# Kernel optimization log

Hardware: AMD Instinct MI355X
Metric: run time of the kernel (lower is better)

The kernel has to match this reference:

```python
import jax, jax.numpy as jnp
import numpy as np

B, N, D_IN = 4, 2048, 768
D_OUT, H = 768, 12
HD = D_OUT // H  # 64


def setup_inputs() -> dict:
    key = jax.random.key(0)
    ks = jax.random.split(key, 6)
    s = 0.02
    return {
        "x": jax.random.normal(ks[0], (B, N, D_IN), dtype=jnp.float32),
        "W_q": jax.random.normal(ks[1], (D_IN, D_OUT), dtype=jnp.float32) * s,
        "W_k": jax.random.normal(ks[2], (D_IN, D_OUT), dtype=jnp.float32) * s,
        "W_v": jax.random.normal(ks[3], (D_IN, D_OUT), dtype=jnp.float32) * s,
        "W_o": jax.random.normal(ks[4], (D_OUT, D_OUT), dtype=jnp.float32) * s,
        "b_o": jax.random.normal(ks[5], (D_OUT,), dtype=jnp.float32) * s,
    }


def reference(x, W_q, W_k, W_v, W_o, b_o):
    b, n, _ = x.shape
    # project and split heads: [b, h, n, hd]
    q = (x @ W_q).reshape(b, n, H, HD).transpose(0, 2, 1, 3)
    k = (x @ W_k).reshape(b, n, H, HD).transpose(0, 2, 1, 3)
    v = (x @ W_v).reshape(b, n, H, HD).transpose(0, 2, 1, 3)
    scores = jnp.einsum("bhqd,bhkd->bhqk", q, k)
    causal = jnp.tril(jnp.ones((n, n), dtype=bool))
    scores = jnp.where(causal, scores, -jnp.inf)
    w = jax.nn.softmax(scores / jnp.sqrt(jnp.float32(HD)), axis=-1)
    ctx = jnp.einsum("bhqk,bhkd->bhqd", w, v)
    ctx = ctx.transpose(0, 2, 1, 3).reshape(b, n, D_OUT)
    return ctx @ W_o + b_o
```

## Files before the change

kernel.cpp:

```cpp
#include <hip/hip_runtime.h>
#include <hip/hip_bf16.h>
#include <stdint.h>

typedef unsigned short u16;
typedef __attribute__((ext_vector_type(8))) short short8;
typedef __attribute__((ext_vector_type(4))) float f32x4;
typedef __attribute__((ext_vector_type(16))) float f32x16;

#define GLOBAL_AS __attribute__((address_space(1)))
#define LDS_AS __attribute__((address_space(3)))

#define BB 4
#define NSEQ 2048
#define DIN 768
#define DOUT 768
#define NH 12
#define HD 64
#define MROWS (BB*NSEQ)

static __device__ __forceinline__ u16 f2bf(float f) {
  union { float f; uint32_t u; } v; v.f = f;
  uint32_t r = (v.u + 0x7fffu + ((v.u >> 16) & 1u)) >> 16;
  return (u16)r;
}
static __device__ __forceinline__ uint32_t pack2b(float lo, float hi) {
  union { __hip_bfloat162 h; uint32_t u; } cv;
  cv.h.x = __float2bfloat16(lo);
  cv.h.y = __float2bfloat16(hi);
  return cv.u;
}

__global__ __launch_bounds__(256) void convert2_k(const float* __restrict__ x,
                          const float* __restrict__ Wq, const float* __restrict__ Wk,
                          const float* __restrict__ Wv, const float* __restrict__ Wo,
                          u16* __restrict__ xb, u16* __restrict__ WqT,
                          u16* __restrict__ WkT, u16* __restrict__ WvT,
                          u16* __restrict__ WoT) {
  int tid = threadIdx.x;
  if (blockIdx.x < 576) {
    int wi = blockIdx.x;
    int which = wi / 144, t = wi % 144;
    int tr = t / 12, tc = t % 12;
    const float* src = which==0 ? Wq : which==1 ? Wk : which==2 ? Wv : Wo;
    u16* dst = which==0 ? WqT : which==1 ? WkT : which==2 ? WvT : WoT;
    __shared__ u16 lt[64][65];
    int r0 = tid >> 6, c = tid & 63;
#pragma unroll
    for (int rr=0; rr<16; rr++) {
      int row = rr*4 + r0;
      lt[row][c] = f2bf(src[(size_t)(tr*64+row)*DOUT + tc*64 + c]);
    }
    __syncthreads();
#pragma unroll
    for (int rr=0; rr<16; rr++) {
      int row = rr*4 + r0;
      dst[(size_t)(tc*64+row)*DIN + tr*64 + c] = lt[c][row];
    }
  } else {
    const float4* x4 = (const float4*)x;
    uint2* o4 = (uint2*)xb;
    int n4 = MROWS*DIN/4;
    int i = (int)(blockIdx.x - 576) * 256 + tid;
    for (; i < n4; i += 2048*256) {
      float4 v = x4[i];
      uint2 o; o.x = pack2b(v.x, v.y); o.y = pack2b(v.z, v.w);
      o4[i] = o;
    }
  }
}

__global__ __launch_bounds__(256) void gemm_qkv_k(const u16* __restrict__ A,
                                                  const u16* __restrict__ Bt,
                                                  u16* __restrict__ Qg,
                                                  u16* __restrict__ Kgo,
                                                  u16* __restrict__ Vto) {
  const int K = DIN;
  int xcd = blockIdx.x & 7, j = blockIdx.x >> 3;
  int m0 = (xcd*8 + (j & 7)) * 128;
  int n0 = (j >> 3) * 128;
  int tid = threadIdx.x;
  int lane = tid & 63, wid = tid >> 6;
  int wr = wid >> 1, wc = wid & 1;
  int g = lane >> 4, r = lane & 15;

  __shared__ __attribute__((aligned(16))) u16 sbuf[128*129];
  u16* lA = sbuf;
  u16* lB = sbuf + 4096;

  f32x4 acc[4][4];
#pragma unroll
  for (int i=0;i<4;i++)
#pragma unroll
    for (int jj=0;jj<4;jj++) acc[i][jj] = (f32x4){0.f,0.f,0.f,0.f};

  for (int k0 = 0; k0 < K; k0 += 32) {
#pragma unroll
    for (int i=0;i<2;i++) {
      int ch = wid*2 + i;
      int e = ch*512 + lane*8;
      int row = e >> 5, col = e & 31;
      __builtin_amdgcn_global_load_lds(
        (GLOBAL_AS void*)(A + (size_t)(m0+row)*K + k0 + col),
        (LDS_AS void*)(&lA[ch*512]), 16, 0, 0);
      __builtin_amdgcn_global_load_lds(
        (GLOBAL_AS void*)(Bt + (size_t)(n0+row)*K + k0 + col),
        (LDS_AS void*)(&lB[ch*512]), 16, 0, 0);
    }
    __syncthreads();
    short8 af[4], bf[4];
#pragma unroll
    for (int f=0; f<4; f++) {
      af[f] = *(const short8*)&lA[(wr*64 + f*16 + r)*32 + g*8];
      bf[f] = *(const short8*)&lB[(wc*64 + f*16 + r)*32 + g*8];
    }
#pragma unroll
    for (int fr=0; fr<4; fr++)
#pragma unroll
      for (int fc=0; fc<4; fc++)
        acc[fr][fc] = __builtin_amdgcn_mfma_f32_16x16x32_bf16(af[fr], bf[fc], acc[fr][fc], 0, 0, 0);
    __syncthreads();
  }

  if (n0 < 1536) {
    bool isQ = n0 < 768;
    u16* outb = isQ ? Qg : Kgo;
    int nb = isQ ? n0 : n0 - 768;
#pragma unroll
    for (int fr=0; fr<4; fr++)
#pragma unroll
      for (int fc=0; fc<4; fc++)
#pragma unroll
        for (int v=0; v<4; v++) {
          int row = m0 + wr*64 + fr*16 + g*4 + v;
          int cc  = nb + wc*64 + fc*16 + r;
          int b = row >> 11, nn = row & (NSEQ-1);
          float val = acc[fr][fc][v];
          if (isQ) val *= 0.18033688f;
          outb[(((size_t)b*NH + (cc>>6))*NSEQ + nn)*HD + (cc&63)] = f2bf(val);
        }
  } else {
    int nb = n0 - 1536;
#pragma unroll
    for (int fr=0; fr<4; fr++)
#pragma unroll
      for (int fc=0; fc<4; fc++)
#pragma unroll
        for (int v=0; v<4; v++) {
          int ii = wr*64 + fr*16 + g*4 + v;
          int jj = wc*64 + fc*16 + r;
          sbuf[ii*129 + jj] = f2bf(acc[fr][fc][v]);
        }
    __syncthreads();
    int b = m0 >> 11;
#pragma unroll 1
    for (int rep=0; rep<64; rep++) {
      int flat = rep*256 + tid;
      int jj = flat >> 7, ii = flat & 127;
      int cc = nb + jj;
      int nn = (m0 + ii) & (NSEQ-1);
      Vto[(((size_t)b*NH + (cc>>6))*HD + (cc&63))*NSEQ + nn] = sbuf[ii*129 + jj];
    }
  }
}

__global__ __launch_bounds__(256) void gemm_o_k(const u16* __restrict__ A,
                                                const u16* __restrict__ Bt,
                                                float* __restrict__ outf,
                                                const float* __restrict__ bias) {
  const int K = DIN;
  int xcd = blockIdx.x & 7, j = blockIdx.x >> 3;
  int m0 = (xcd*8 + (j & 7)) * 128;
  int n0 = (j >> 3) * 128;
  int tid = threadIdx.x;
  int lane = tid & 63, wid = tid >> 6;
  int wr = wid >> 1, wc = wid & 1;
  int g = lane >> 4, r = lane & 15;

  __shared__ __attribute__((aligned(16))) u16 lA[128*32];
  __shared__ __attribute__((aligned(16))) u16 lB[128*32];

  f32x4 acc[4][4];
#pragma unroll
  for (int i=0;i<4;i++)
#pragma unroll
    for (int jj=0;jj<4;jj++) acc[i][jj] = (f32x4){0.f,0.f,0.f,0.f};

  for (int k0 = 0; k0 < K; k0 += 32) {
#pragma unroll
    for (int i=0;i<2;i++) {
      int ch = wid*2 + i;
      int e = ch*512 + lane*8;
      int row = e >> 5, col = e & 31;
      __builtin_amdgcn_global_load_lds(
        (GLOBAL_AS void*)(A + (size_t)(m0+row)*K + k0 + col),
        (LDS_AS void*)(&lA[ch*512]), 16, 0, 0);
      __builtin_amdgcn_global_load_lds(
        (GLOBAL_AS void*)(Bt + (size_t)(n0+row)*K + k0 + col),
        (LDS_AS void*)(&lB[ch*512]), 16, 0, 0);
    }
    __syncthreads();
    short8 af[4], bf[4];
#pragma unroll
    for (int f=0; f<4; f++) {
      af[f] = *(const short8*)&lA[(wr*64 + f*16 + r)*32 + g*8];
      bf[f] = *(const short8*)&lB[(wc*64 + f*16 + r)*32 + g*8];
    }
#pragma unroll
    for (int fr=0; fr<4; fr++)
#pragma unroll
      for (int fc=0; fc<4; fc++)
        acc[fr][fc] = __builtin_amdgcn_mfma_f32_16x16x32_bf16(af[fr], bf[fc], acc[fr][fc], 0, 0, 0);
    __syncthreads();
  }

#pragma unroll
  for (int fr=0; fr<4; fr++)
#pragma unroll
    for (int fc=0; fc<4; fc++)
#pragma unroll
      for (int v=0; v<4; v++) {
        int row = m0 + wr*64 + fr*16 + g*4 + v;
        int cc  = n0 + wc*64 + fc*16 + r;
        outf[(size_t)row*DOUT + cc] = acc[fr][fc][v] + bias[cc];
      }
}

__global__ __launch_bounds__(256, 4) void attn7_k(const u16* __restrict__ Q,
                                                  const u16* __restrict__ Kg,
                                                  const u16* __restrict__ Vt,
                                                  u16* __restrict__ ctx) {
  int i = blockIdx.x;
  int xcd = i & 7, j = i >> 3;
  int bh = xcd * 6 + (j >> 5);
  int chunk = 31 - (j & 31);
  int nkt = chunk + 1;
  int lane = threadIdx.x & 63;
  int w = threadIdx.x >> 6;
  int p = w >> 1;
  int ch = w & 1;
  int col = lane & 31;
  int hi = lane >> 5;
  int sw = (col & 7) << 4;

  const u16* Qb = Q  + (size_t)bh * NSEQ * HD;
  const u16* Kb = Kg + (size_t)bh * NSEQ * HD;
  const u16* Vb = Vt + (size_t)bh * HD * NSEQ;

  __shared__ __attribute__((aligned(16))) char smem[2][16384];

  auto stage = [&](int buf, int k0) {
#pragma unroll
    for (int ii=0; ii<2; ii++) {
      int cb = (w*2+ii) * 1024;
      int d  = cb + lane*16;
      int row = d >> 7;
      int src = (d & 127) ^ ((row & 7) << 4);
      __builtin_amdgcn_global_load_lds(
        (GLOBAL_AS void*)((const char*)Kb + (size_t)(k0+row)*128 + src),
        (LDS_AS void*)(&smem[buf][cb]), 16, 0, 0);
      __builtin_amdgcn_global_load_lds(
        (GLOBAL_AS void*)((const char*)Vb + (size_t)row*(NSEQ*2) + (size_t)k0*2 + src),
        (LDS_AS void*)(&smem[buf][8192+cb]), 16, 0, 0);
    }
  };

  int qw0 = chunk*64 + p*32;
  int q = qw0 + col;

  short8 qf[4];
#pragma unroll
  for (int ksl = 0; ksl < 4; ksl++)
    qf[ksl] = *(const short8*)&Qb[(size_t)q * HD + ksl*16 + hi*8];

  short8 ones8;
#pragma unroll
  for (int z=0; z<8; z++) ones8[z] = (short)0x3F80;

  f32x16 od[2], ol;
#pragma unroll
  for (int z=0; z<16; z++) { od[0][z] = 0.f; od[1][z] = 0.f; ol[z] = 0.f; }

  stage(0, 0);

#pragma unroll 1
  for (int t = 0; t < nkt; t++) {
    asm volatile("s_waitcnt vmcnt(0)" ::: "memory");
    __builtin_amdgcn_s_barrier();
    asm volatile("" ::: "memory");

    if (t + 1 < nkt) stage((t+1) & 1, (t+1)*64);

    int k0c = t*64 + ch*32;
    if (k0c <= qw0 + 31) {
      const char* Kt = &smem[t & 1][0];
      const char* Vtile = &smem[t & 1][8192];
      f32x16 s;
#pragma unroll
      for (int z=0; z<16; z++) s[z] = 0.f;
#pragma unroll
      for (int ksl=0; ksl<4; ksl++) {
        short8 kf = *(const short8*)(Kt + (ch*32+col)*128 + ((ksl*32 + hi*16) ^ sw));
        s = __builtin_amdgcn_mfma_f32_32x32x16_bf16(kf, qf[ksl], s, 0, 0, 0);
      }
      if (k0c + 31 > qw0) {
#pragma unroll
        for (int r2=0; r2<16; r2++) {
          int kv = k0c + (r2&3) + 8*(r2>>2) + 4*hi;
          if (kv > q) s[r2] = -1e30f;
        }
      }
      uint32_t a[8];
#pragma unroll
      for (int ww=0; ww<8; ww++) {
        float p0 = __builtin_amdgcn_exp2f(s[2*ww]);
        float p1 = __builtin_amdgcn_exp2f(s[2*ww+1]);
        a[ww] = pack2b(p0, p1);
      }

      uint32_t b[8];
#pragma unroll
      for (int ww=0; ww<8; ww++) b[ww] = (uint32_t)__shfl_xor((int)a[ww], 32);
      union { uint32_t wdat[4]; short8 s8; } u0, u1;
      u0.wdat[0] = hi ? b[2]   : a[0];
      u0.wdat[1] = hi ? b[3]   : a[1];
      u0.wdat[2] = hi ? a[2]   : b[0];
      u0.wdat[3] = hi ? a[3]   : b[1];
      u1.wdat[0] = hi ? b[6]   : a[4];
      u1.wdat[1] = hi ? b[7]   : a[5];
      u1.wdat[2] = hi ? a[6]   : b[4];
      u1.wdat[3] = hi ? a[7]   : b[5];
#pragma unroll
      for (int dc=0; dc<2; dc++) {
        short8 vf0 = *(const short8*)(Vtile + (dc*32+col)*128 + ((ch*64 + hi*16) ^ sw));
        od[dc] = __builtin_amdgcn_mfma_f32_32x32x16_bf16(vf0, u0.s8, od[dc], 0, 0, 0);
        short8 vf1 = *(const short8*)(Vtile + (dc*32+col)*128 + ((ch*64 + 32 + hi*16) ^ sw));
        od[dc] = __builtin_amdgcn_mfma_f32_32x32x16_bf16(vf1, u1.s8, od[dc], 0, 0, 0);
      }
      ol = __builtin_amdgcn_mfma_f32_32x32x16_bf16(ones8, u0.s8, ol, 0, 0, 0);
      ol = __builtin_amdgcn_mfma_f32_32x32x16_bf16(ones8, u1.s8, ol, 0, 0, 0);
    }
  }
  __syncthreads();

  float* mg = (float*)&smem[0][0] + p * (33*64);
  if (ch) {
#pragma unroll
    for (int dc=0; dc<2; dc++)
#pragma unroll
      for (int jj=0; jj<16; jj++) mg[(dc*16+jj)*64 + lane] = od[dc][jj];
    mg[32*64 + lane] = ol[0];
  }
  __syncthreads();
  if (!ch) {
    float inv = 1.0f / (ol[0] + mg[32*64 + lane]);
    int b = bh / NH, h = bh % NH;
    u16* cp_ = ctx + ((size_t)b * NSEQ + q) * DOUT + h * HD;
#pragma unroll
    for (int dc=0; dc<2; dc++)
#pragma unroll
      for (int t4=0; t4<4; t4++) {
        int d0 = dc*32 + t4*8 + hi*4;
        float v0 = (od[dc][t4*4+0] + mg[(dc*16+t4*4+0)*64 + lane]) * inv;
        float v1 = (od[dc][t4*4+1] + mg[(dc*16+t4*4+1)*64 + lane]) * inv;
        float v2 = (od[dc][t4*4+2] + mg[(dc*16+t4*4+2)*64 + lane]) * inv;
        float v3 = (od[dc][t4*4+3] + mg[(dc*16+t4*4+3)*64 + lane]) * inv;
        *(uint32_t*)(cp_ + d0)     = pack2b(v0, v1);
        *(uint32_t*)(cp_ + d0 + 2) = pack2b(v2, v3);
      }
  }
}

extern "C" void kernel_launch(void* const* d_in, const int* in_sizes, int n_in,
                              void* d_out, int out_size, void* d_ws, size_t ws_size,
                              hipStream_t stream) {
  const float* x   = (const float*)d_in[0];
  const float* Wq  = (const float*)d_in[1];
  const float* Wk  = (const float*)d_in[2];
  const float* Wv  = (const float*)d_in[3];
  const float* Wo  = (const float*)d_in[4];
  const float* bo  = (const float*)d_in[5];
  float* out = (float*)d_out;

  u16* ws  = (u16*)d_ws;
  u16* xb  = ws;
  u16* WqT = xb  + (size_t)MROWS*DIN;
  u16* WkT = WqT + (size_t)DIN*DOUT;
  u16* WvT = WkT + (size_t)DIN*DOUT;
  u16* WoT = WvT + (size_t)DIN*DOUT;
  u16* Qg  = WoT + (size_t)DIN*DOUT;
  u16* Kg  = Qg  + (size_t)MROWS*DOUT;
  u16* Vt  = Kg  + (size_t)MROWS*DOUT;
  u16* ctx = Vt  + (size_t)MROWS*DOUT;

  convert2_k<<<2624, 256, 0, stream>>>(x, Wq, Wk, Wv, Wo, xb, WqT, WkT, WvT, WoT);

  gemm_qkv_k<<<1152, 256, 0, stream>>>(xb, WqT, Qg, Kg, Vt);

  attn7_k<<<1536, 256, 0, stream>>>(Qg, Kg, Vt, ctx);

  gemm_o_k<<<384, 256, 0, stream>>>(ctx, WoT, out, bo);
}
```

Measured before the change: 142.3 us.

## Double-buffer LDS tiles in QKV and output GEMMs, interleave QKV column tiles

Both projection GEMMs now use two LDS buffers, issuing global-to-LDS loads for the next K-slice before computing on the current one, with one barrier per iteration instead of two. The aim is to overlap memory latency with MFMA work. The QKV GEMM also remaps its column-tile index so Q, K and V tiles are interleaved across blocks, which may balance the different epilogues (V is transposed) across the schedule. The cost is doubled LDS footprint for staging, which may reduce occupancy. Correctness depends on the single barrier plus vmcnt wait ordering LDS reuse properly.

```diff
diff --git a/kernel.cpp b/kernel.cpp
--- a/kernel.cpp
+++ b/kernel.cpp
@@ -77,7 +77,9 @@
   const int K = DIN;
   int xcd = blockIdx.x & 7, j = blockIdx.x >> 3;
   int m0 = (xcd*8 + (j & 7)) * 128;
-  int n0 = (j >> 3) * 128;
+  int nt = j >> 3;
+  nt = (nt % 3) * 6 + nt / 3;
+  int n0 = nt * 128;
   int tid = threadIdx.x;
   int lane = tid & 63, wid = tid >> 6;
   int wr = wid >> 1, wc = wid & 1;
@@ -85,15 +87,9 @@
 
   __shared__ __attribute__((aligned(16))) u16 sbuf[128*129];
   u16* lA = sbuf;
-  u16* lB = sbuf + 4096;
-
-  f32x4 acc[4][4];
-#pragma unroll
-  for (int i=0;i<4;i++)
-#pragma unroll
-    for (int jj=0;jj<4;jj++) acc[i][jj] = (f32x4){0.f,0.f,0.f,0.f};
-
-  for (int k0 = 0; k0 < K; k0 += 32) {
+  u16* lB = sbuf + 8192;
+
+  auto stage = [&](int buf, int k0) {
 #pragma unroll
     for (int i=0;i<2;i++) {
       int ch = wid*2 + i;
@@ -101,25 +97,41 @@
       int row = e >> 5, col = e & 31;
       __builtin_amdgcn_global_load_lds(
         (GLOBAL_AS void*)(A + (size_t)(m0+row)*K + k0 + col),
-        (LDS_AS void*)(&lA[ch*512]), 16, 0, 0);
+        (LDS_AS void*)(&lA[buf*4096 + ch*512]), 16, 0, 0);
       __builtin_amdgcn_global_load_lds(
         (GLOBAL_AS void*)(Bt + (size_t)(n0+row)*K + k0 + col),
-        (LDS_AS void*)(&lB[ch*512]), 16, 0, 0);
-    }
-    __syncthreads();
+        (LDS_AS void*)(&lB[buf*4096 + ch*512]), 16, 0, 0);
+    }
+  };
+
+  f32x4 acc[4][4];
+#pragma unroll
+  for (int i=0;i<4;i++)
+#pragma unroll
+    for (int jj=0;jj<4;jj++) acc[i][jj] = (f32x4){0.f,0.f,0.f,0.f};
+
+  stage(0, 0);
+  int buf = 0;
+  for (int k0 = 0; k0 < K; k0 += 32) {
+    asm volatile("s_waitcnt vmcnt(0)" ::: "memory");
+    __builtin_amdgcn_s_barrier();
+    asm volatile("" ::: "memory");
+    if (k0 + 32 < K) stage(buf ^ 1, k0 + 32);
+
     short8 af[4], bf[4];
 #pragma unroll
     for (int f=0; f<4; f++) {
-      af[f] = *(const short8*)&lA[(wr*64 + f*16 + r)*32 + g*8];
-      bf[f] = *(const short8*)&lB[(wc*64 + f*16 + r)*32 + g*8];
+      af[f] = *(const short8*)&lA[buf*4096 + (wr*64 + f*16 + r)*32 + g*8];
+      bf[f] = *(const short8*)&lB[buf*4096 + (wc*64 + f*16 + r)*32 + g*8];
     }
 #pragma unroll
     for (int fr=0; fr<4; fr++)
 #pragma unroll
       for (int fc=0; fc<4; fc++)
         acc[fr][fc] = __builtin_amdgcn_mfma_f32_16x16x32_bf16(af[fr], bf[fc], acc[fr][fc], 0, 0, 0);
-    __syncthreads();
-  }
+    buf ^= 1;
+  }
+  __syncthreads();
 
   if (n0 < 1536) {
     bool isQ = n0 < 768;
@@ -176,16 +188,10 @@
   int wr = wid >> 1, wc = wid & 1;
   int g = lane >> 4, r = lane & 15;
 
-  __shared__ __attribute__((aligned(16))) u16 lA[128*32];
-  __shared__ __attribute__((aligned(16))) u16 lB[128*32];
-
-  f32x4 acc[4][4];
-#pragma unroll
-  for (int i=0;i<4;i++)
-#pragma unroll
-    for (int jj=0;jj<4;jj++) acc[i][jj] = (f32x4){0.f,0.f,0.f,0.f};
-
-  for (int k0 = 0; k0 < K; k0 += 32) {
+  __shared__ __attribute__((aligned(16))) u16 lA[2][4096];
+  __shared__ __attribute__((aligned(16))) u16 lB[2][4096];
+
+  auto stage = [&](int buf, int k0) {
 #pragma unroll
     for (int i=0;i<2;i++) {
       int ch = wid*2 + i;
@@ -193,24 +199,39 @@
       int row = e >> 5, col = e & 31;
       __builtin_amdgcn_global_load_lds(
         (GLOBAL_AS void*)(A + (size_t)(m0+row)*K + k0 + col),
-        (LDS_AS void*)(&lA[ch*512]), 16, 0, 0);
+        (LDS_AS void*)(&lA[buf][ch*512]), 16, 0, 0);
       __builtin_amdgcn_global_load_lds(
         (GLOBAL_AS void*)(Bt + (size_t)(n0+row)*K + k0 + col),
-        (LDS_AS void*)(&lB[ch*512]), 16, 0, 0);
-    }
-    __syncthreads();
+        (LDS_AS void*)(&lB[buf][ch*512]), 16, 0, 0);
+    }
+  };
+
+  f32x4 acc[4][4];
+#pragma unroll
+  for (int i=0;i<4;i++)
+#pragma unroll
+    for (int jj=0;jj<4;jj++) acc[i][jj] = (f32x4){0.f,0.f,0.f,0.f};
+
+  stage(0, 0);
+  int buf = 0;
+  for (int k0 = 0; k0 < K; k0 += 32) {
+    asm volatile("s_waitcnt vmcnt(0)" ::: "memory");
+    __builtin_amdgcn_s_barrier();
+    asm volatile("" ::: "memory");
+    if (k0 + 32 < K) stage(buf ^ 1, k0 + 32);
+
     short8 af[4], bf[4];
 #pragma unroll
     for (int f=0; f<4; f++) {
-      af[f] = *(const short8*)&lA[(wr*64 + f*16 + r)*32 + g*8];
-      bf[f] = *(const short8*)&lB[(wc*64 + f*16 + r)*32 + g*8];
+      af[f] = *(const short8*)&lA[buf][(wr*64 + f*16 + r)*32 + g*8];
+      bf[f] = *(const short8*)&lB[buf][(wc*64 + f*16 + r)*32 + g*8];
     }
 #pragma unroll
     for (int fr=0; fr<4; fr++)
 #pragma unroll
       for (int fc=0; fc<4; fc++)
         acc[fr][fc] = __builtin_amdgcn_mfma_f32_16x16x32_bf16(af[fr], bf[fc], acc[fr][fc], 0, 0, 0);
-    __syncthreads();
+    buf ^= 1;
   }
 
 #pragma unroll
```

After: 136.4 us. -4.1%, faster.
